# Kernel tuning notes

Hardware: AMD Instinct MI355X
Metric: run time of the kernel (lower is better)

Reference implementation:

```python
import jax, jax.numpy as jnp
import numpy as np

N_BLOCKS = 500000
BLOCK_DIM = 64


def setup_inputs() -> dict:
    key = jax.random.key(0)
    ks = jax.random.split(key, 7)
    d = BLOCK_DIM
    s = jax.random.normal(ks[0], (d,), dtype=jnp.float32)
    h = jax.random.normal(ks[1], (N_BLOCKS * d,), dtype=jnp.float32)
    keys = jax.random.normal(ks[2], (N_BLOCKS, d), dtype=jnp.float32)
    # xavier-uniform style scale for d x d matrices
    lim = np.sqrt(6.0 / (d + d)).astype(np.float32)
    U = jax.random.uniform(ks[3], (d, d), dtype=jnp.float32, minval=-lim, maxval=lim)
    V = jax.random.uniform(ks[4], (d, d), dtype=jnp.float32, minval=-lim, maxval=lim)
    W = jax.random.uniform(ks[5], (d, d), dtype=jnp.float32, minval=-lim, maxval=lim)
    bias = jnp.full((d,), 0.001, dtype=jnp.float32)
    prelu_a = jnp.array([0.25], dtype=jnp.float32)  # nn.PReLU() default
    return {"s": s, "h": h, "keys": keys, "U": U, "V": V, "W": W,
            "bias": bias, "prelu_a": prelu_a}


def reference(s, h, keys, U, V, W, bias, prelu_a):
    d = s.shape[0]
    hb = h.reshape(-1, d)                      # [N, d] blocks of h
    # gate: sigmoid(<s,hj> + <s,wj>) per block
    g = jax.nn.sigmoid(hb @ s + keys @ s)      # [N]
    # candidate: PReLU(U hj + V wj + W s + b), batched over blocks
    pre = hb @ U.T + keys @ V.T + (W @ s) + bias  # [N, d]
    act = jnp.where(pre >= 0, pre, prelu_a[0] * pre)
    h_new = hb + g[:, None] * act              # gated residual update
    h_new = h_new / jnp.linalg.norm(h_new, axis=1, keepdims=True)
    return h_new.reshape(-1)
```

## Files before the change

### kernel.cpp

```cpp
#include <hip/hip_runtime.h>

#define D 64
#define ROWS 64
#define TPB 256

typedef float f4 __attribute__((ext_vector_type(4)));
typedef short s8 __attribute__((ext_vector_type(8)));

static __device__ __forceinline__ unsigned short f2bf(float x) {
  union { float f; unsigned u; } v; v.f = x;
  return (unsigned short)((v.u + 0x7FFFu + ((v.u >> 16) & 1u)) >> 16);
}

static __device__ __forceinline__ s8 pack8(f4 a, f4 b) {
  s8 r;
  r[0] = (short)f2bf(a.x); r[1] = (short)f2bf(a.y);
  r[2] = (short)f2bf(a.z); r[3] = (short)f2bf(a.w);
  r[4] = (short)f2bf(b.x); r[5] = (short)f2bf(b.y);
  r[6] = (short)f2bf(b.z); r[7] = (short)f2bf(b.w);
  return r;
}

static __device__ __forceinline__ f4 fma4s(float a, f4 b, f4 c) {
  f4 r;
  r.x = fmaf(a, b.x, c.x);
  r.y = fmaf(a, b.y, c.y);
  r.z = fmaf(a, b.z, c.z);
  r.w = fmaf(a, b.w, c.w);
  return r;
}

static __device__ __forceinline__ f4 prelu4(f4 p, float a) {
  f4 r;
  r.x = p.x >= 0.0f ? p.x : a * p.x;
  r.y = p.y >= 0.0f ? p.y : a * p.y;
  r.z = p.z >= 0.0f ? p.z : a * p.z;
  r.w = p.w >= 0.0f ? p.w : a * p.w;
  return r;
}

static __device__ __forceinline__ float dot4(f4 x, f4 y, f4 z, float acc) {
  acc = fmaf(x.x + y.x, z.x, acc);
  acc = fmaf(x.y + y.y, z.y, acc);
  acc = fmaf(x.z + y.z, z.z, acc);
  acc = fmaf(x.w + y.w, z.w, acc);
  return acc;
}

__global__ __launch_bounds__(TPB, 4) void dmc_fused(
    const float* __restrict__ h,
    const float* __restrict__ keys,
    const float* __restrict__ s,
    const float* __restrict__ U,
    const float* __restrict__ V,
    const float* __restrict__ W,
    const float* __restrict__ bias,
    const float* __restrict__ prelu_a,
    float* __restrict__ out,
    const int nblocks) {
  __shared__ __align__(16) unsigned short Ub[D * D];
  __shared__ __align__(16) unsigned short Vb[D * D];
  __shared__ __align__(16) float cc[D];

  const int tid  = threadIdx.x;
  const int lane = tid & 63;
  const int wv   = tid >> 6;
  const int g    = lane >> 4;
  const int rl   = lane & 15;
  const int r    = wv * 16 + rl;
  const int j0   = blockIdx.x * ROWS;
  const int nrem = nblocks - j0;
  const int rc   = (r < nrem) ? r : (nrem - 1);

  const f4* __restrict__ hrow = reinterpret_cast<const f4*>(h + (size_t)(j0 + rc) * D);
  const f4* __restrict__ krow = reinterpret_cast<const f4*>(keys + (size_t)(j0 + rc) * D);
  const f4 ph0a = hrow[2 * g];      const f4 ph0b = hrow[2 * g + 1];
  const f4 ph1a = hrow[8 + 2 * g];  const f4 ph1b = hrow[8 + 2 * g + 1];
  const f4 pk0a = krow[2 * g];      const f4 pk0b = krow[2 * g + 1];
  const f4 pk1a = krow[8 + 2 * g];  const f4 pk1b = krow[8 + 2 * g + 1];
  const f4 hr0 = hrow[0 + g];
  const f4 hr1 = hrow[4 + g];
  const f4 hr2 = hrow[8 + g];
  const f4 hr3 = hrow[12 + g];
  __builtin_amdgcn_sched_barrier(0);

  const f4* __restrict__ Ug = reinterpret_cast<const f4*>(U);
  const f4* __restrict__ Vg = reinterpret_cast<const f4*>(V);
  s8* __restrict__ Ub8w = reinterpret_cast<s8*>(Ub);
  s8* __restrict__ Vb8w = reinterpret_cast<s8*>(Vb);
  #pragma unroll
  for (int t = 0; t < 2; ++t) {
    const int m  = tid + TPB * t;
    const int c  = m >> 3;
    const int sl = m & 7;
    Ub8w[c * 8 + (sl ^ (c & 7))] = pack8(Ug[c * 16 + sl * 2], Ug[c * 16 + sl * 2 + 1]);
    Vb8w[c * 8 + (sl ^ (c & 7))] = pack8(Vg[c * 16 + sl * 2], Vg[c * 16 + sl * 2 + 1]);
  }

  if (tid < D) {
    const f4* __restrict__ wr = reinterpret_cast<const f4*>(W + tid * D);
    const f4* __restrict__ sr = reinterpret_cast<const f4*>(s);
    float acc = bias[tid];
    #pragma unroll
    for (int q = 0; q < 16; ++q) {
      const f4 wq = wr[q];
      const f4 sq = sr[q];
      acc = fmaf(wq.x, sq.x, acc);
      acc = fmaf(wq.y, sq.y, acc);
      acc = fmaf(wq.z, sq.z, acc);
      acc = fmaf(wq.w, sq.w, acc);
    }
    cc[tid] = acc;
  }
  __syncthreads();

  const f4* __restrict__ sg4 = reinterpret_cast<const f4*>(s);
  float gd = dot4(ph0a, pk0a, sg4[2 * g], 0.0f);
  gd = dot4(ph0b, pk0b, sg4[2 * g + 1], gd);
  gd = dot4(ph1a, pk1a, sg4[8 + 2 * g], gd);
  gd = dot4(ph1b, pk1b, sg4[8 + 2 * g + 1], gd);
  const s8 bh0 = pack8(ph0a, ph0b);
  const s8 bh1 = pack8(ph1a, ph1b);
  const s8 bk0 = pack8(pk0a, pk0b);
  const s8 bk1 = pack8(pk1a, pk1b);

  const f4* __restrict__ cc4 = reinterpret_cast<const f4*>(cc);
  f4 acc0 = cc4[0 + g];
  f4 acc1 = cc4[4 + g];
  f4 acc2 = cc4[8 + g];
  f4 acc3 = cc4[12 + g];

  const s8* __restrict__ Ub8 = reinterpret_cast<const s8*>(Ub);
  const s8* __restrict__ Vb8 = reinterpret_cast<const s8*>(Vb);
  #pragma unroll
  for (int ks = 0; ks < 2; ++ks) {
    const int asl = ks * 4 + g;
    const s8 bh = (ks == 0) ? bh0 : bh1;
    const s8 bk = (ks == 0) ? bk0 : bk1;
    const int c0i = 0 * 16 + rl, c1i = 1 * 16 + rl;
    const int c2i = 2 * 16 + rl, c3i = 3 * 16 + rl;
    const s8 au0 = Ub8[c0i * 8 + (asl ^ (c0i & 7))];
    const s8 au1 = Ub8[c1i * 8 + (asl ^ (c1i & 7))];
    const s8 au2 = Ub8[c2i * 8 + (asl ^ (c2i & 7))];
    const s8 au3 = Ub8[c3i * 8 + (asl ^ (c3i & 7))];
    const s8 av0 = Vb8[c0i * 8 + (asl ^ (c0i & 7))];
    const s8 av1 = Vb8[c1i * 8 + (asl ^ (c1i & 7))];
    const s8 av2 = Vb8[c2i * 8 + (asl ^ (c2i & 7))];
    const s8 av3 = Vb8[c3i * 8 + (asl ^ (c3i & 7))];
    acc0 = __builtin_amdgcn_mfma_f32_16x16x32_bf16(au0, bh, acc0, 0, 0, 0);
    acc1 = __builtin_amdgcn_mfma_f32_16x16x32_bf16(au1, bh, acc1, 0, 0, 0);
    acc2 = __builtin_amdgcn_mfma_f32_16x16x32_bf16(au2, bh, acc2, 0, 0, 0);
    acc3 = __builtin_amdgcn_mfma_f32_16x16x32_bf16(au3, bh, acc3, 0, 0, 0);
    acc0 = __builtin_amdgcn_mfma_f32_16x16x32_bf16(av0, bk, acc0, 0, 0, 0);
    acc1 = __builtin_amdgcn_mfma_f32_16x16x32_bf16(av1, bk, acc1, 0, 0, 0);
    acc2 = __builtin_amdgcn_mfma_f32_16x16x32_bf16(av2, bk, acc2, 0, 0, 0);
    acc3 = __builtin_amdgcn_mfma_f32_16x16x32_bf16(av3, bk, acc3, 0, 0, 0);
  }

  gd += __shfl_xor(gd, 16);
  gd += __shfl_xor(gd, 32);
  const float gt = 1.0f / (1.0f + __expf(-gd));
  const float a  = prelu_a[0];

  f4 o0 = fma4s(gt, prelu4(acc0, a), hr0);
  f4 o1 = fma4s(gt, prelu4(acc1, a), hr1);
  f4 o2 = fma4s(gt, prelu4(acc2, a), hr2);
  f4 o3 = fma4s(gt, prelu4(acc3, a), hr3);

  float ss = o0.x * o0.x + o0.y * o0.y + o0.z * o0.z + o0.w * o0.w;
  ss = fmaf(o1.x, o1.x, ss); ss = fmaf(o1.y, o1.y, ss);
  ss = fmaf(o1.z, o1.z, ss); ss = fmaf(o1.w, o1.w, ss);
  ss = fmaf(o2.x, o2.x, ss); ss = fmaf(o2.y, o2.y, ss);
  ss = fmaf(o2.z, o2.z, ss); ss = fmaf(o2.w, o2.w, ss);
  ss = fmaf(o3.x, o3.x, ss); ss = fmaf(o3.y, o3.y, ss);
  ss = fmaf(o3.z, o3.z, ss); ss = fmaf(o3.w, o3.w, ss);
  ss += __shfl_xor(ss, 16);
  ss += __shfl_xor(ss, 32);
  const float rn = rsqrtf(ss);

  if (r < nrem) {
    float* __restrict__ orow = out + (size_t)(j0 + r) * D + g * 4;
    *reinterpret_cast<f4*>(orow +  0) = o0 * rn;
    *reinterpret_cast<f4*>(orow + 16) = o1 * rn;
    *reinterpret_cast<f4*>(orow + 32) = o2 * rn;
    *reinterpret_cast<f4*>(orow + 48) = o3 * rn;
  }
}

extern "C" void kernel_launch(void* const* d_in, const int* in_sizes, int n_in,
                              void* d_out, int out_size, void* d_ws, size_t ws_size,
                              hipStream_t stream) {
  const float* s       = (const float*)d_in[0];
  const float* h       = (const float*)d_in[1];
  const float* keys    = (const float*)d_in[2];
  const float* U       = (const float*)d_in[3];
  const float* V       = (const float*)d_in[4];
  const float* W       = (const float*)d_in[5];
  const float* bias    = (const float*)d_in[6];
  const float* prelu_a = (const float*)d_in[7];
  float* out = (float*)d_out;

  const int nblocks = in_sizes[1] / D;
  const int grid = (nblocks + ROWS - 1) / ROWS;
  dmc_fused<<<grid, TPB, 0, stream>>>(h, keys, s, U, V, W, bias, prelu_a, out,
                                      nblocks);
}
```

Measured before the change: 103.1 us.

## Process two row tiles per workgroup to amortize U/V/W setup

Each workgroup now handles two 64-row tiles instead of one. It issues global loads for both tiles up front, then converts U/V to bf16 in LDS and computes W·s+bias once, and applies both to the two tiles. This halves the per-row cost of loading the shared weights and of the barrier, and puts more memory loads in flight per thread. The trade-off is higher register pressure, with launch bounds lowered to 3 waves per EU, and half as many workgroups.

Measured after the change: 119.4 us. 1.16x slower.

```diff
diff --git a/kernel.cpp b/kernel.cpp
--- a/kernel.cpp
+++ b/kernel.cpp
@@ -47,91 +47,29 @@
   return acc;
 }
 
-__global__ __launch_bounds__(TPB, 4) void dmc_fused(
-    const float* __restrict__ h,
-    const float* __restrict__ keys,
-    const float* __restrict__ s,
-    const float* __restrict__ U,
-    const float* __restrict__ V,
-    const float* __restrict__ W,
-    const float* __restrict__ bias,
-    const float* __restrict__ prelu_a,
-    float* __restrict__ out,
-    const int nblocks) {
-  __shared__ __align__(16) unsigned short Ub[D * D];
-  __shared__ __align__(16) unsigned short Vb[D * D];
-  __shared__ __align__(16) float cc[D];
-
-  const int tid  = threadIdx.x;
-  const int lane = tid & 63;
-  const int wv   = tid >> 6;
-  const int g    = lane >> 4;
-  const int rl   = lane & 15;
-  const int r    = wv * 16 + rl;
-  const int j0   = blockIdx.x * ROWS;
-  const int nrem = nblocks - j0;
-  const int rc   = (r < nrem) ? r : (nrem - 1);
-
-  const f4* __restrict__ hrow = reinterpret_cast<const f4*>(h + (size_t)(j0 + rc) * D);
-  const f4* __restrict__ krow = reinterpret_cast<const f4*>(keys + (size_t)(j0 + rc) * D);
-  const f4 ph0a = hrow[2 * g];      const f4 ph0b = hrow[2 * g + 1];
-  const f4 ph1a = hrow[8 + 2 * g];  const f4 ph1b = hrow[8 + 2 * g + 1];
-  const f4 pk0a = krow[2 * g];      const f4 pk0b = krow[2 * g + 1];
-  const f4 pk1a = krow[8 + 2 * g];  const f4 pk1b = krow[8 + 2 * g + 1];
-  const f4 hr0 = hrow[0 + g];
-  const f4 hr1 = hrow[4 + g];
-  const f4 hr2 = hrow[8 + g];
-  const f4 hr3 = hrow[12 + g];
-  __builtin_amdgcn_sched_barrier(0);
-
-  const f4* __restrict__ Ug = reinterpret_cast<const f4*>(U);
-  const f4* __restrict__ Vg = reinterpret_cast<const f4*>(V);
-  s8* __restrict__ Ub8w = reinterpret_cast<s8*>(Ub);
-  s8* __restrict__ Vb8w = reinterpret_cast<s8*>(Vb);
-  #pragma unroll
-  for (int t = 0; t < 2; ++t) {
-    const int m  = tid + TPB * t;
-    const int c  = m >> 3;
-    const int sl = m & 7;
-    Ub8w[c * 8 + (sl ^ (c & 7))] = pack8(Ug[c * 16 + sl * 2], Ug[c * 16 + sl * 2 + 1]);
-    Vb8w[c * 8 + (sl ^ (c & 7))] = pack8(Vg[c * 16 + sl * 2], Vg[c * 16 + sl * 2 + 1]);
-  }
-
-  if (tid < D) {
-    const f4* __restrict__ wr = reinterpret_cast<const f4*>(W + tid * D);
-    const f4* __restrict__ sr = reinterpret_cast<const f4*>(s);
-    float acc = bias[tid];
-    #pragma unroll
-    for (int q = 0; q < 16; ++q) {
-      const f4 wq = wr[q];
-      const f4 sq = sr[q];
-      acc = fmaf(wq.x, sq.x, acc);
-      acc = fmaf(wq.y, sq.y, acc);
-      acc = fmaf(wq.z, sq.z, acc);
-      acc = fmaf(wq.w, sq.w, acc);
-    }
-    cc[tid] = acc;
-  }
-  __syncthreads();
-
-  const f4* __restrict__ sg4 = reinterpret_cast<const f4*>(s);
-  float gd = dot4(ph0a, pk0a, sg4[2 * g], 0.0f);
-  gd = dot4(ph0b, pk0b, sg4[2 * g + 1], gd);
-  gd = dot4(ph1a, pk1a, sg4[8 + 2 * g], gd);
-  gd = dot4(ph1b, pk1b, sg4[8 + 2 * g + 1], gd);
+static __device__ __forceinline__ void consume_tile(
+    const int j0, const int nrem, const int r, const int g, const int rl,
+    const f4 ph0a, const f4 ph0b, const f4 ph1a, const f4 ph1b,
+    const f4 pk0a, const f4 pk0b, const f4 pk1a, const f4 pk1b,
+    const f4 hr0, const f4 hr1, const f4 hr2, const f4 hr3,
+    const f4 sA0, const f4 sA1, const f4 sB0, const f4 sB1,
+    const s8* __restrict__ Ub8, const s8* __restrict__ Vb8,
+    const f4* __restrict__ cc4, const float a,
+    float* __restrict__ out) {
+  float gd = dot4(ph0a, pk0a, sA0, 0.0f);
+  gd = dot4(ph0b, pk0b, sA1, gd);
+  gd = dot4(ph1a, pk1a, sB0, gd);
+  gd = dot4(ph1b, pk1b, sB1, gd);
   const s8 bh0 = pack8(ph0a, ph0b);
   const s8 bh1 = pack8(ph1a, ph1b);
   const s8 bk0 = pack8(pk0a, pk0b);
   const s8 bk1 = pack8(pk1a, pk1b);
 
-  const f4* __restrict__ cc4 = reinterpret_cast<const f4*>(cc);
   f4 acc0 = cc4[0 + g];
   f4 acc1 = cc4[4 + g];
   f4 acc2 = cc4[8 + g];
   f4 acc3 = cc4[12 + g];
 
-  const s8* __restrict__ Ub8 = reinterpret_cast<const s8*>(Ub);
-  const s8* __restrict__ Vb8 = reinterpret_cast<const s8*>(Vb);
   #pragma unroll
   for (int ks = 0; ks < 2; ++ks) {
     const int asl = ks * 4 + g;
@@ -160,7 +98,6 @@
   gd += __shfl_xor(gd, 16);
   gd += __shfl_xor(gd, 32);
   const float gt = 1.0f / (1.0f + __expf(-gd));
-  const float a  = prelu_a[0];
 
   f4 o0 = fma4s(gt, prelu4(acc0, a), hr0);
   f4 o1 = fma4s(gt, prelu4(acc1, a), hr1);
@@ -184,6 +121,120 @@
     *reinterpret_cast<f4*>(orow + 16) = o1 * rn;
     *reinterpret_cast<f4*>(orow + 32) = o2 * rn;
     *reinterpret_cast<f4*>(orow + 48) = o3 * rn;
+  }
+}
+
+__global__ __launch_bounds__(TPB, 3) void dmc_fused(
+    const float* __restrict__ h,
+    const float* __restrict__ keys,
+    const float* __restrict__ s,
+    const float* __restrict__ U,
+    const float* __restrict__ V,
+    const float* __restrict__ W,
+    const float* __restrict__ bias,
+    const float* __restrict__ prelu_a,
+    float* __restrict__ out,
+    const int nblocks,
+    const int ntiles) {
+  __shared__ __align__(16) unsigned short Ub[D * D];
+  __shared__ __align__(16) unsigned short Vb[D * D];
+  __shared__ __align__(16) float cc[D];
+
+  const int tid  = threadIdx.x;
+  const int lane = tid & 63;
+  const int wv   = tid >> 6;
+  const int g    = lane >> 4;
+  const int rl   = lane & 15;
+  const int r    = wv * 16 + rl;
+
+  const int tA = blockIdx.x * 2;
+  const int tB = tA + 1;
+  const bool hasB = (tB < ntiles);
+
+  const int j0A = tA * ROWS;
+  const int nremA = nblocks - j0A;
+  const int rcA = (r < nremA) ? r : (nremA - 1);
+  const f4* __restrict__ hrA = reinterpret_cast<const f4*>(h + (size_t)(j0A + rcA) * D);
+  const f4* __restrict__ krA = reinterpret_cast<const f4*>(keys + (size_t)(j0A + rcA) * D);
+  const f4 Ah0a = hrA[2 * g];      const f4 Ah0b = hrA[2 * g + 1];
+  const f4 Ah1a = hrA[8 + 2 * g];  const f4 Ah1b = hrA[8 + 2 * g + 1];
+  const f4 Ak0a = krA[2 * g];      const f4 Ak0b = krA[2 * g + 1];
+  const f4 Ak1a = krA[8 + 2 * g];  const f4 Ak1b = krA[8 + 2 * g + 1];
+  const f4 Ar0 = hrA[0 + g];
+  const f4 Ar1 = hrA[4 + g];
+  const f4 Ar2 = hrA[8 + g];
+  const f4 Ar3 = hrA[12 + g];
+
+  f4 Bh0a = {0,0,0,0}, Bh0b = Bh0a, Bh1a = Bh0a, Bh1b = Bh0a;
+  f4 Bk0a = Bh0a, Bk0b = Bh0a, Bk1a = Bh0a, Bk1b = Bh0a;
+  f4 Br0 = Bh0a, Br1 = Bh0a, Br2 = Bh0a, Br3 = Bh0a;
+  int j0B = 0, nremB = 0;
+  if (hasB) {
+    j0B = tB * ROWS;
+    nremB = nblocks - j0B;
+    const int rcB = (r < nremB) ? r : (nremB - 1);
+    const f4* __restrict__ hrB = reinterpret_cast<const f4*>(h + (size_t)(j0B + rcB) * D);
+    const f4* __restrict__ krB = reinterpret_cast<const f4*>(keys + (size_t)(j0B + rcB) * D);
+    Bh0a = hrB[2 * g];      Bh0b = hrB[2 * g + 1];
+    Bh1a = hrB[8 + 2 * g];  Bh1b = hrB[8 + 2 * g + 1];
+    Bk0a = krB[2 * g];      Bk0b = krB[2 * g + 1];
+    Bk1a = krB[8 + 2 * g];  Bk1b = krB[8 + 2 * g + 1];
+    Br0 = hrB[0 + g];
+    Br1 = hrB[4 + g];
+    Br2 = hrB[8 + g];
+    Br3 = hrB[12 + g];
+  }
+  __builtin_amdgcn_sched_barrier(0);
+
+  const f4* __restrict__ Ug = reinterpret_cast<const f4*>(U);
+  const f4* __restrict__ Vg = reinterpret_cast<const f4*>(V);
+  s8* __restrict__ Ub8w = reinterpret_cast<s8*>(Ub);
+  s8* __restrict__ Vb8w = reinterpret_cast<s8*>(Vb);
+  #pragma unroll
+  for (int t = 0; t < 2; ++t) {
+    const int m  = tid + TPB * t;
+    const int c  = m >> 3;
+    const int sl = m & 7;
+    Ub8w[c * 8 + (sl ^ (c & 7))] = pack8(Ug[c * 16 + sl * 2], Ug[c * 16 + sl * 2 + 1]);
+    Vb8w[c * 8 + (sl ^ (c & 7))] = pack8(Vg[c * 16 + sl * 2], Vg[c * 16 + sl * 2 + 1]);
+  }
+
+  if (tid < D) {
+    const f4* __restrict__ wr = reinterpret_cast<const f4*>(W + tid * D);
+    const f4* __restrict__ sr = reinterpret_cast<const f4*>(s);
+    float acc = bias[tid];
+    #pragma unroll
+    for (int q = 0; q < 16; ++q) {
+      const f4 wq = wr[q];
+      const f4 sq = sr[q];
+      acc = fmaf(wq.x, sq.x, acc);
+      acc = fmaf(wq.y, sq.y, acc);
+      acc = fmaf(wq.z, sq.z, acc);
+      acc = fmaf(wq.w, sq.w, acc);
+    }
+    cc[tid] = acc;
+  }
+  __syncthreads();
+
+  const f4* __restrict__ sg4 = reinterpret_cast<const f4*>(s);
+  const f4 sA0 = sg4[2 * g];
+  const f4 sA1 = sg4[2 * g + 1];
+  const f4 sB0 = sg4[8 + 2 * g];
+  const f4 sB1 = sg4[8 + 2 * g + 1];
+  const float a = prelu_a[0];
+  const s8* __restrict__ Ub8 = reinterpret_cast<const s8*>(Ub);
+  const s8* __restrict__ Vb8 = reinterpret_cast<const s8*>(Vb);
+  const f4* __restrict__ cc4 = reinterpret_cast<const f4*>(cc);
+
+  consume_tile(j0A, nremA, r, g, rl,
+               Ah0a, Ah0b, Ah1a, Ah1b, Ak0a, Ak0b, Ak1a, Ak1b,
+               Ar0, Ar1, Ar2, Ar3, sA0, sA1, sB0, sB1,
+               Ub8, Vb8, cc4, a, out);
+  if (hasB) {
+    consume_tile(j0B, nremB, r, g, rl,
+                 Bh0a, Bh0b, Bh1a, Bh1b, Bk0a, Bk0b, Bk1a, Bk1b,
+                 Br0, Br1, Br2, Br3, sA0, sA1, sB0, sB1,
+                 Ub8, Vb8, cc4, a, out);
   }
 }
 
@@ -201,7 +252,8 @@
   float* out = (float*)d_out;
 
   const int nblocks = in_sizes[1] / D;
-  const int grid = (nblocks + ROWS - 1) / ROWS;
+  const int ntiles  = (nblocks + ROWS - 1) / ROWS;
+  const int grid    = (ntiles + 1) / 2;
   dmc_fused<<<grid, TPB, 0, stream>>>(h, keys, s, U, V, W, bias, prelu_a, out,
-                                      nblocks);
-}
+                                      nblocks, ntiles);
+}
```
